# Kernel optimization log

Hardware: AMD Instinct MI355X
Metric: run time of the kernel (lower is better)

The kernel has to match this reference:

```python
import jax, jax.numpy as jnp
import numpy as np

E = 1024   # embedding_size
K = 64     # key_size
DH = 64    # head_size
H = 16     # layer_size (num heads)
F = 4096   # hidden_size
B, S = 4, 2048
EPS = float(np.finfo(np.float32).eps)  # torch RMSNorm default eps


def setup_inputs() -> dict:
    key = jax.random.key(0)
    ks = jax.random.split(key, 12)
    embeddings = jax.random.normal(ks[0], (B, S, E), dtype=jnp.float32)
    # causal additive mask: 0 on/below diagonal, -1e9 above
    tri = jnp.triu(jnp.ones((S, S), dtype=bool), k=1)
    causal_buffer = jnp.where(tri, -1e9, 0.0).astype(jnp.float32)[None]  # [1,S,S]
    # standard RoPE cos/sin buffers over the key dim
    inv_freq = 1.0 / (10000.0 ** (jnp.arange(0, K // 2, dtype=jnp.float32) * 2.0 / K))
    ang = jnp.arange(S, dtype=jnp.float32)[:, None] * inv_freq[None, :]  # [S,K/2]
    ang = jnp.concatenate([ang, ang], axis=-1)                           # [S,K]
    cos_buffer = jnp.cos(ang)[None]  # [1,S,K]
    sin_buffer = jnp.sin(ang)[None]
    sc = 0.02
    wq = jax.random.normal(ks[1], (H, E, K), dtype=jnp.float32) * sc
    wk = jax.random.normal(ks[2], (H, E, K), dtype=jnp.float32) * sc
    wv = jax.random.normal(ks[3], (H, E, DH), dtype=jnp.float32) * sc
    w_proj = jax.random.normal(ks[4], (E, E), dtype=jnp.float32) * sc
    attn_norm_w = jnp.ones((E,), dtype=jnp.float32)
    mlp_norm_w = jnp.ones((E,), dtype=jnp.float32)
    w_up = jax.random.normal(ks[5], (E, F), dtype=jnp.float32) * sc
    w_gate = jax.random.normal(ks[6], (E, F), dtype=jnp.float32) * sc
    w_down = jax.random.normal(ks[7], (F, E), dtype=jnp.float32) * sc
    return {"embeddings": embeddings, "causal_buffer": causal_buffer,
            "cos_buffer": cos_buffer, "sin_buffer": sin_buffer,
            "wq": wq, "wk": wk, "wv": wv, "w_proj": w_proj,
            "attn_norm_w": attn_norm_w, "mlp_norm_w": mlp_norm_w,
            "w_up": w_up, "w_gate": w_gate, "w_down": w_down}


def _rmsnorm(x, w):
    ms = jnp.mean(x * x, axis=-1, keepdims=True)
    return x * jax.lax.rsqrt(ms + EPS) * w


def _rotate(x, cos, sin):
    # x: [B,H,S,K]; cos/sin: [1,1,S,K]. swapped = cat(second_half, first_half)
    swapped = jnp.concatenate([x[..., K // 2:], x[..., :K // 2]], axis=-1)
    return cos * x + sin * swapped


def reference(embeddings, causal_buffer, cos_buffer, sin_buffer,
              wq, wk, wv, w_proj, attn_norm_w, mlp_norm_w,
              w_up, w_gate, w_down):
    cos = cos_buffer[:, None]  # [1,1,S,K]
    sin = sin_buffer[:, None]
    # NOTE: original computes attention_norm(embeddings) but feeds RAW
    # embeddings to the heads; we reproduce that faithfully.
    q = _rotate(jnp.einsum('bse,hek->bhsk', embeddings, wq), cos, sin)
    k = _rotate(jnp.einsum('bse,hek->bhsk', embeddings, wk), cos, sin)
    v = jnp.einsum('bse,hed->bhsd', embeddings, wv)
    scores = jnp.einsum('bhsk,bhtk->bhst', q, k) / jnp.sqrt(jnp.float32(K))
    scores = scores + causal_buffer[:, None]  # broadcast over heads
    weights = jax.nn.softmax(scores, axis=-1)
    attn = jnp.einsum('bhst,bhtd->bhsd', weights, v)  # [B,H,S,DH]
    attn = attn.transpose(0, 2, 1, 3).reshape(attn.shape[0], attn.shape[2], H * DH)
    x = embeddings + attn @ w_proj
    h = _rmsnorm(x, mlp_norm_w)
    mlp = (h @ w_up) * jax.nn.elu(h @ w_gate)
    return x + mlp @ w_down
```

## Files before the change

### kernel.cpp

```cpp
#include <hip/hip_runtime.h>
#include <cstdint>
#include <cstddef>

#define E_DIM 1024
#define S_LEN 2048
#define NB 4
#define NH 16
#define F_DIM 4096

typedef __attribute__((ext_vector_type(8))) __bf16 bf16x8;
typedef __attribute__((ext_vector_type(4))) __bf16 bf16x4;
typedef __attribute__((ext_vector_type(4))) float f32x4;

__device__ __forceinline__ f32x4 mfma16(bf16x8 a, bf16x8 b, f32x4 c) {
  return __builtin_amdgcn_mfma_f32_16x16x32_bf16(a, b, c, 0, 0, 0);
}

__device__ __forceinline__ unsigned short f2bf(float f) {
  __bf16 h = (__bf16)f;
  return __builtin_bit_cast(unsigned short, h);
}

__device__ __forceinline__ void gl_lds16(const void* gptr, void* lptr) {
  __builtin_amdgcn_global_load_lds(
      (const __attribute__((address_space(1))) void*)gptr,
      (__attribute__((address_space(3))) void*)lptr, 16, 0, 0);
}


__global__ __launch_bounds__(256) void cast_emb_kernel(
    const float4* __restrict__ in, ushort4* __restrict__ out) {
  int i = blockIdx.x * 256 + threadIdx.x;
  float4 v = in[i];
  ushort4 o;
  o.x = f2bf(v.x); o.y = f2bf(v.y); o.z = f2bf(v.z); o.w = f2bf(v.w);
  out[i] = o;
}

__global__ __launch_bounds__(256) void transpose_cast_kernel(
    const float* __restrict__ in, unsigned short* __restrict__ out, int R, int C) {
  __shared__ float tile[32][33];
  const int bz = blockIdx.z;
  const float* ip = in + (size_t)bz * R * C;
  const int r0 = blockIdx.y * 32, c0 = blockIdx.x * 32;
  const int tc = threadIdx.x & 31, tr = threadIdx.x >> 5;
#pragma unroll
  for (int i = 0; i < 4; ++i)
    tile[tr + i * 8][tc] = ip[(size_t)(r0 + tr + i * 8) * C + (c0 + tc)];
  __syncthreads();
#pragma unroll
  for (int i = 0; i < 4; ++i)
    out[(size_t)(bz * C + c0 + tr + i * 8) * R + (r0 + tc)] = f2bf(tile[tc][tr + i * 8]);
}

template <int EPI>
__global__ __launch_bounds__(256) void gemm_bt(
    const unsigned short* __restrict__ A, const unsigned short* __restrict__ Bt,
    int Kd, int N,
    const float* __restrict__ aux, const float* __restrict__ cosb,
    const float* __restrict__ sinb,
    unsigned short* __restrict__ qout, unsigned short* __restrict__ kout,
    unsigned short* __restrict__ vtout, float* __restrict__ fout) {
  __shared__ unsigned short As[128 * 32];
  __shared__ unsigned short Bs[128 * 32];
  const int t = threadIdx.x;
  const int lane = t & 63, w = t >> 6;
  const int quad = lane >> 4, l15 = lane & 15;
  const int wm = (w >> 1) * 64, wn = (w & 1) * 64;
  const int m0 = blockIdx.y * 128, n0 = blockIdx.x * 128;
  const int r = t >> 2, cb = (t & 3) * 8;
  const unsigned short* ga = A + (size_t)(m0 + r) * Kd + cb;
  const unsigned short* gb = Bt + (size_t)(n0 + r) * Kd + cb;
  unsigned short* lA0 = &As[r * 32 + cb];
  unsigned short* lA1 = &As[(r + 64) * 32 + cb];
  unsigned short* lB0 = &Bs[r * 32 + cb];
  unsigned short* lB1 = &Bs[(r + 64) * 32 + cb];
  f32x4 acc[4][4] = {};
  for (int k0 = 0; k0 < Kd; k0 += 32) {
    __syncthreads();
    gl_lds16(ga + k0, lA0);
    gl_lds16(ga + (size_t)64 * Kd + k0, lA1);
    gl_lds16(gb + k0, lB0);
    gl_lds16(gb + (size_t)64 * Kd + k0, lB1);
    __syncthreads();
    bf16x8 af[4], bfr[4];
#pragma unroll
    for (int mi = 0; mi < 4; ++mi)
      af[mi] = *reinterpret_cast<const bf16x8*>(&As[(wm + mi * 16 + l15) * 32 + quad * 8]);
#pragma unroll
    for (int ni = 0; ni < 4; ++ni)
      bfr[ni] = *reinterpret_cast<const bf16x8*>(&Bs[(wn + ni * 16 + l15) * 32 + quad * 8]);
#pragma unroll
    for (int mi = 0; mi < 4; ++mi)
#pragma unroll
      for (int ni = 0; ni < 4; ++ni)
        acc[mi][ni] = mfma16(af[mi], bfr[ni], acc[mi][ni]);
  }
  if (EPI == 0) {
#pragma unroll
    for (int mi = 0; mi < 4; ++mi) {
      const int mbase = m0 + wm + mi * 16 + quad * 4;
#pragma unroll
      for (int nt = 0; nt < 4; ++nt) {
        const int n = n0 + wn + nt * 16 + l15;
        const int seg = n >> 10, rest = n & 1023, hh = rest >> 6, kk = rest & 63;
#pragma unroll
        for (int rg = 0; rg < 4; ++rg) {
          const int m = mbase + rg;
          const int b = m >> 11, s = m & 2047;
          const float v = acc[mi][nt][rg];
          if (seg == 2) {
            vtout[(((size_t)(b * NH + hh)) * 64 + kk) * S_LEN + s] = f2bf(v);
          } else {
            const float sw = acc[mi][nt ^ 2][rg];
            const float cv = cosb[s * 64 + kk], sv = sinb[s * 64 + kk];
            const float scl = (seg == 0) ? 0.125f : 1.0f;
            unsigned short* dst = (seg == 0) ? qout : kout;
            dst[(((size_t)(b * NH + hh)) * S_LEN + s) * 64 + kk] = f2bf((cv * v + sv * sw) * scl);
          }
        }
      }
    }
  } else {
#pragma unroll
    for (int mi = 0; mi < 4; ++mi) {
      const int mbase = m0 + wm + mi * 16 + quad * 4;
#pragma unroll
      for (int nt = 0; nt < 4; ++nt) {
        const int n = n0 + wn + nt * 16 + l15;
#pragma unroll
        for (int rg = 0; rg < 4; ++rg) {
          const size_t idx = (size_t)(mbase + rg) * 1024 + n;
          fout[idx] = aux[idx] + acc[mi][nt][rg];
        }
      }
    }
  }
}

__global__ __launch_bounds__(256) void gemm_upgate(
    const unsigned short* __restrict__ A, const unsigned short* __restrict__ Bu,
    const unsigned short* __restrict__ Bg, unsigned short* __restrict__ gout) {
  __shared__ unsigned short As[128 * 32];
  __shared__ unsigned short Us[64 * 32];
  __shared__ unsigned short Gs[64 * 32];
  const int Kd = 1024;
  const int t = threadIdx.x;
  const int lane = t & 63, w = t >> 6;
  const int quad = lane >> 4, l15 = lane & 15;
  const int wm = (w >> 1) * 64, wn = (w & 1) * 32;
  const int m0 = blockIdx.y * 128, n0 = blockIdx.x * 64;
  const int r = t >> 2, cb = (t & 3) * 8;
  const unsigned short* ga = A + (size_t)(m0 + r) * Kd + cb;
  const unsigned short* gu = Bu + (size_t)(n0 + r) * Kd + cb;
  const unsigned short* gg = Bg + (size_t)(n0 + r) * Kd + cb;
  f32x4 au[4][2] = {}, ag[4][2] = {};
  for (int k0 = 0; k0 < Kd; k0 += 32) {
    __syncthreads();
    gl_lds16(ga + k0, &As[r * 32 + cb]);
    gl_lds16(ga + (size_t)64 * Kd + k0, &As[(r + 64) * 32 + cb]);
    gl_lds16(gu + k0, &Us[r * 32 + cb]);
    gl_lds16(gg + k0, &Gs[r * 32 + cb]);
    __syncthreads();
    bf16x8 af[4], bu[2], bg[2];
#pragma unroll
    for (int mi = 0; mi < 4; ++mi)
      af[mi] = *reinterpret_cast<const bf16x8*>(&As[(wm + mi * 16 + l15) * 32 + quad * 8]);
#pragma unroll
    for (int ni = 0; ni < 2; ++ni) {
      bu[ni] = *reinterpret_cast<const bf16x8*>(&Us[(wn + ni * 16 + l15) * 32 + quad * 8]);
      bg[ni] = *reinterpret_cast<const bf16x8*>(&Gs[(wn + ni * 16 + l15) * 32 + quad * 8]);
    }
#pragma unroll
    for (int mi = 0; mi < 4; ++mi)
#pragma unroll
      for (int ni = 0; ni < 2; ++ni) {
        au[mi][ni] = mfma16(af[mi], bu[ni], au[mi][ni]);
        ag[mi][ni] = mfma16(af[mi], bg[ni], ag[mi][ni]);
      }
  }
#pragma unroll
  for (int mi = 0; mi < 4; ++mi) {
    const int mbase = m0 + wm + mi * 16 + quad * 4;
#pragma unroll
    for (int ni = 0; ni < 2; ++ni) {
      const int n = n0 + wn + ni * 16 + l15;
#pragma unroll
      for (int rg = 0; rg < 4; ++rg) {
        const float u = au[mi][ni][rg], gt = ag[mi][ni][rg];
        const float e = gt > 0.f ? gt : (__expf(gt) - 1.f);
        gout[(size_t)(mbase + rg) * F_DIM + n] = f2bf(u * e);
      }
    }
  }
}

#define PS_STRIDE 68
__global__ __launch_bounds__(256) void flash_attn(
    const unsigned short* __restrict__ qb, const unsigned short* __restrict__ kb,
    const unsigned short* __restrict__ vtb, unsigned short* __restrict__ attn) {
  __shared__ unsigned short Ks[64 * 64];
  __shared__ unsigned short Vts[64 * 64];
  __shared__ unsigned short Ps[128 * PS_STRIDE];
  const int t = threadIdx.x, lane = t & 63, w = t >> 6;
  const int quad = lane >> 4, l15 = lane & 15;
  const int qt = 15 - blockIdx.y;
  const int bh = blockIdx.x;
  const int b = bh >> 4, hh = bh & 15;
  const unsigned short* qg = qb + (size_t)bh * S_LEN * 64;
  const unsigned short* kg = kb + (size_t)bh * S_LEN * 64;
  const unsigned short* vg = vtb + (size_t)bh * 64 * S_LEN;
  bf16x8 aq[2][2];
#pragma unroll
  for (int mi = 0; mi < 2; ++mi)
#pragma unroll
    for (int ks = 0; ks < 2; ++ks)
      aq[mi][ks] = *reinterpret_cast<const bf16x8*>(
          qg + (size_t)(qt * 128 + w * 32 + mi * 16 + l15) * 64 + ks * 32 + quad * 8);
  f32x4 o[2][4] = {};
  float lpart[2][4] = {};
  const int ktmax = 2 * qt + 1;
  for (int kt = 0; kt <= ktmax; ++kt) {
    __syncthreads();
    {
      const int rk = t >> 3, ck = (t & 7) * 8;
#pragma unroll
      for (int i = 0; i < 2; ++i) {
        gl_lds16(kg + (size_t)(kt * 64 + rk + i * 32) * 64 + ck, &Ks[(rk + i * 32) * 64 + ck]);
        gl_lds16(vg + (size_t)(rk + i * 32) * S_LEN + kt * 64 + ck, &Vts[(rk + i * 32) * 64 + ck]);
      }
    }
    __syncthreads();
    f32x4 sacc[2][4];
#pragma unroll
    for (int mi = 0; mi < 2; ++mi)
#pragma unroll
      for (int nt = 0; nt < 4; ++nt) sacc[mi][nt] = (f32x4){-8.f, -8.f, -8.f, -8.f};
#pragma unroll
    for (int nt = 0; nt < 4; ++nt) {
      bf16x8 b0 = *reinterpret_cast<const bf16x8*>(&Ks[(nt * 16 + l15) * 64 + quad * 8]);
      bf16x8 b1 = *reinterpret_cast<const bf16x8*>(&Ks[(nt * 16 + l15) * 64 + 32 + quad * 8]);
#pragma unroll
      for (int mi = 0; mi < 2; ++mi) {
        sacc[mi][nt] = mfma16(aq[mi][0], b0, sacc[mi][nt]);
        sacc[mi][nt] = mfma16(aq[mi][1], b1, sacc[mi][nt]);
      }
    }
    if (kt >= 2 * qt) {
#pragma unroll
      for (int mi = 0; mi < 2; ++mi)
#pragma unroll
        for (int nt = 0; nt < 4; ++nt)
#pragma unroll
          for (int rg = 0; rg < 4; ++rg) {
            const int row = qt * 128 + w * 32 + mi * 16 + quad * 4 + rg;
            const int col = kt * 64 + nt * 16 + l15;
            if (col > row) sacc[mi][nt][rg] = -1e9f;
          }
    }
#pragma unroll
    for (int mi = 0; mi < 2; ++mi)
#pragma unroll
      for (int nt = 0; nt < 4; ++nt)
#pragma unroll
        for (int rg = 0; rg < 4; ++rg) {
          const float p = __expf(sacc[mi][nt][rg]);
          lpart[mi][rg] += p;
          Ps[(w * 32 + mi * 16 + quad * 4 + rg) * PS_STRIDE + nt * 16 + l15] = f2bf(p);
        }
#pragma unroll
    for (int ks = 0; ks < 2; ++ks) {
      bf16x8 ap[2];
#pragma unroll
      for (int mi = 0; mi < 2; ++mi) {
        const unsigned short* pp =
            &Ps[(w * 32 + mi * 16 + l15) * PS_STRIDE + ks * 32 + quad * 8];
        bf16x4 lo = *reinterpret_cast<const bf16x4*>(pp);
        bf16x4 hi = *reinterpret_cast<const bf16x4*>(pp + 4);
        ap[mi] = __builtin_shufflevector(lo, hi, 0, 1, 2, 3, 4, 5, 6, 7);
      }
#pragma unroll
      for (int vt = 0; vt < 4; ++vt) {
        bf16x8 bv = *reinterpret_cast<const bf16x8*>(
            &Vts[(vt * 16 + l15) * 64 + ks * 32 + quad * 8]);
#pragma unroll
        for (int mi = 0; mi < 2; ++mi) o[mi][vt] = mfma16(ap[mi], bv, o[mi][vt]);
      }
    }
  }
  float linv[2][4];
#pragma unroll
  for (int mi = 0; mi < 2; ++mi)
#pragma unroll
    for (int rg = 0; rg < 4; ++rg) {
      float rs = lpart[mi][rg];
#pragma unroll
      for (int d = 1; d < 16; d <<= 1) rs += __shfl_xor(rs, d);
      linv[mi][rg] = 1.0f / rs;
    }
#pragma unroll
  for (int mi = 0; mi < 2; ++mi)
#pragma unroll
    for (int vt = 0; vt < 4; ++vt)
#pragma unroll
      for (int rg = 0; rg < 4; ++rg) {
        const int row = w * 32 + mi * 16 + quad * 4 + rg;
        const int s = qt * 128 + row;
        const float ov = o[mi][vt][rg] * linv[mi][rg];
        attn[((size_t)(b * S_LEN + s)) * E_DIM + hh * 64 + vt * 16 + l15] = f2bf(ov);
      }
}

__global__ __launch_bounds__(256) void rmsnorm_kernel(
    const float* __restrict__ x, const float* __restrict__ wgt,
    unsigned short* __restrict__ hout) {
  const int row = blockIdx.x;
  const int t = threadIdx.x;
  const float4 v = reinterpret_cast<const float4*>(x + (size_t)row * E_DIM)[t];
  float ss = v.x * v.x + v.y * v.y + v.z * v.z + v.w * v.w;
#pragma unroll
  for (int d = 1; d < 64; d <<= 1) ss += __shfl_xor(ss, d);
  __shared__ float red[4];
  if ((t & 63) == 0) red[t >> 6] = ss;
  __syncthreads();
  const float tot = red[0] + red[1] + red[2] + red[3];
  const float sc = rsqrtf(tot * (1.f / 1024.f) + 1.1920929e-07f);
  const float4 g = reinterpret_cast<const float4*>(wgt)[t];
  ushort4 ov;
  ov.x = f2bf(v.x * sc * g.x);
  ov.y = f2bf(v.y * sc * g.y);
  ov.z = f2bf(v.z * sc * g.z);
  ov.w = f2bf(v.w * sc * g.w);
  reinterpret_cast<ushort4*>(hout + (size_t)row * E_DIM)[t] = ov;
}

extern "C" void kernel_launch(void* const* d_in, const int* in_sizes, int n_in,
                              void* d_out, int out_size, void* d_ws, size_t ws_size,
                              hipStream_t stream) {
  (void)in_sizes; (void)n_in; (void)out_size; (void)ws_size;
  const float* emb = (const float*)d_in[0];
  const float* cosb = (const float*)d_in[2];
  const float* sinb = (const float*)d_in[3];
  const float* wq = (const float*)d_in[4];
  const float* wk = (const float*)d_in[5];
  const float* wv = (const float*)d_in[6];
  const float* wproj = (const float*)d_in[7];
  const float* mlpw = (const float*)d_in[9];
  const float* wup = (const float*)d_in[10];
  const float* wgate = (const float*)d_in[11];
  const float* wdown = (const float*)d_in[12];
  float* out = (float*)d_out;
  char* ws = (char*)d_ws;
  unsigned short* wqkv_t = (unsigned short*)(ws + 0);
  unsigned short* wproj_t = (unsigned short*)(ws + 6291456);
  unsigned short* wup_t = (unsigned short*)(ws + 8388608);
  unsigned short* wgate_t = (unsigned short*)(ws + 16777216);
  unsigned short* wdown_t = (unsigned short*)(ws + 25165824);
  unsigned short* embb = (unsigned short*)(ws + 33554432);
  unsigned short* qbuf = (unsigned short*)(ws + 50331648);
  unsigned short* kbuf = (unsigned short*)(ws + 67108864);
  unsigned short* vtbuf = (unsigned short*)(ws + 83886080);
  unsigned short* gbuf = (unsigned short*)(ws + 33554432);
  unsigned short* attnb = (unsigned short*)(ws + 100663296);
  float* xbuf = (float*)(ws + 117440512);
  unsigned short* hbuf = (unsigned short*)(ws + 150994944);

  dim3 blk(256);
  cast_emb_kernel<<<8192, blk, 0, stream>>>((const float4*)emb, (ushort4*)embb);
  transpose_cast_kernel<<<dim3(2, 32, 16), blk, 0, stream>>>(wq, wqkv_t, 1024, 64);
  transpose_cast_kernel<<<dim3(2, 32, 16), blk, 0, stream>>>(wk, wqkv_t + 1024 * 1024, 1024, 64);
  transpose_cast_kernel<<<dim3(2, 32, 16), blk, 0, stream>>>(wv, wqkv_t + 2048 * 1024, 1024, 64);
  transpose_cast_kernel<<<dim3(32, 32, 1), blk, 0, stream>>>(wproj, wproj_t, 1024, 1024);
  transpose_cast_kernel<<<dim3(128, 32, 1), blk, 0, stream>>>(wup, wup_t, 1024, 4096);
  transpose_cast_kernel<<<dim3(128, 32, 1), blk, 0, stream>>>(wgate, wgate_t, 1024, 4096);
  transpose_cast_kernel<<<dim3(32, 128, 1), blk, 0, stream>>>(wdown, wdown_t, 4096, 1024);
  gemm_bt<0><<<dim3(24, 64), blk, 0, stream>>>(embb, wqkv_t, 1024, 3072, nullptr, cosb,
                                               sinb, qbuf, kbuf, vtbuf, nullptr);
  flash_attn<<<dim3(64, 16), blk, 0, stream>>>(qbuf, kbuf, vtbuf, attnb);
  gemm_bt<1><<<dim3(8, 64), blk, 0, stream>>>(attnb, wproj_t, 1024, 1024, emb, nullptr,
                                              nullptr, nullptr, nullptr, nullptr, xbuf);
  rmsnorm_kernel<<<8192, blk, 0, stream>>>(xbuf, mlpw, hbuf);
  gemm_upgate<<<dim3(64, 64), blk, 0, stream>>>(hbuf, wup_t, wgate_t, gbuf);
  gemm_bt<2><<<dim3(8, 64), blk, 0, stream>>>(gbuf, wdown_t, 4096, 1024, xbuf, nullptr,
                                              nullptr, nullptr, nullptr, nullptr, out);
}
```

Before: 660.0 us.

## Widen GEMM K-tile to 64 and XOR-swizzle LDS layout in GEMMs and attention

The GEMM kernels now stage 64-wide K slices instead of 32, halving the number of barrier pairs per K loop. Global-to-LDS loads also use an XOR swizzle on 16-byte column chunks (global column permuted by row&7), and all LDS fragment reads apply the matching swizzle to avoid bank conflicts. The same swizzle is applied to the K and V^T tiles in the attention kernel. LDS use per block doubles for the GEMMs, which may reduce occupancy.

```diff
diff --git a/kernel.cpp b/kernel.cpp
--- a/kernel.cpp
+++ b/kernel.cpp
@@ -61,40 +61,46 @@
     const float* __restrict__ sinb,
     unsigned short* __restrict__ qout, unsigned short* __restrict__ kout,
     unsigned short* __restrict__ vtout, float* __restrict__ fout) {
-  __shared__ unsigned short As[128 * 32];
-  __shared__ unsigned short Bs[128 * 32];
+  __shared__ unsigned short As[128 * 64];
+  __shared__ unsigned short Bs[128 * 64];
   const int t = threadIdx.x;
   const int lane = t & 63, w = t >> 6;
   const int quad = lane >> 4, l15 = lane & 15;
   const int wm = (w >> 1) * 64, wn = (w & 1) * 64;
   const int m0 = blockIdx.y * 128, n0 = blockIdx.x * 128;
-  const int r = t >> 2, cb = (t & 3) * 8;
-  const unsigned short* ga = A + (size_t)(m0 + r) * Kd + cb;
-  const unsigned short* gb = Bt + (size_t)(n0 + r) * Kd + cb;
-  unsigned short* lA0 = &As[r * 32 + cb];
-  unsigned short* lA1 = &As[(r + 64) * 32 + cb];
-  unsigned short* lB0 = &Bs[r * 32 + cb];
-  unsigned short* lB1 = &Bs[(r + 64) * 32 + cb];
+  const int sr = t >> 3, sc = t & 7;
+  const int gcoff = (sc ^ (sr & 7)) * 8;
+  const unsigned short* ga = A + (size_t)(m0 + sr) * Kd + gcoff;
+  const unsigned short* gb = Bt + (size_t)(n0 + sr) * Kd + gcoff;
+  unsigned short* lA = &As[sr * 64 + sc * 8];
+  unsigned short* lB = &Bs[sr * 64 + sc * 8];
+  const int xh = l15 & 7;
   f32x4 acc[4][4] = {};
-  for (int k0 = 0; k0 < Kd; k0 += 32) {
-    __syncthreads();
-    gl_lds16(ga + k0, lA0);
-    gl_lds16(ga + (size_t)64 * Kd + k0, lA1);
-    gl_lds16(gb + k0, lB0);
-    gl_lds16(gb + (size_t)64 * Kd + k0, lB1);
-    __syncthreads();
-    bf16x8 af[4], bfr[4];
-#pragma unroll
-    for (int mi = 0; mi < 4; ++mi)
-      af[mi] = *reinterpret_cast<const bf16x8*>(&As[(wm + mi * 16 + l15) * 32 + quad * 8]);
-#pragma unroll
-    for (int ni = 0; ni < 4; ++ni)
-      bfr[ni] = *reinterpret_cast<const bf16x8*>(&Bs[(wn + ni * 16 + l15) * 32 + quad * 8]);
-#pragma unroll
-    for (int mi = 0; mi < 4; ++mi)
+  for (int k0 = 0; k0 < Kd; k0 += 64) {
+    __syncthreads();
+#pragma unroll
+    for (int i = 0; i < 4; ++i) {
+      gl_lds16(ga + (size_t)(i * 32) * Kd + k0, lA + i * 32 * 64);
+      gl_lds16(gb + (size_t)(i * 32) * Kd + k0, lB + i * 32 * 64);
+    }
+    __syncthreads();
+#pragma unroll
+    for (int ks = 0; ks < 2; ++ks) {
+      bf16x8 af[4], bfr[4];
+#pragma unroll
+      for (int mi = 0; mi < 4; ++mi)
+        af[mi] = *reinterpret_cast<const bf16x8*>(
+            &As[(wm + mi * 16 + l15) * 64 + (((ks * 4 + quad) ^ xh) * 8)]);
 #pragma unroll
       for (int ni = 0; ni < 4; ++ni)
-        acc[mi][ni] = mfma16(af[mi], bfr[ni], acc[mi][ni]);
+        bfr[ni] = *reinterpret_cast<const bf16x8*>(
+            &Bs[(wn + ni * 16 + l15) * 64 + (((ks * 4 + quad) ^ xh) * 8)]);
+#pragma unroll
+      for (int mi = 0; mi < 4; ++mi)
+#pragma unroll
+        for (int ni = 0; ni < 4; ++ni)
+          acc[mi][ni] = mfma16(af[mi], bfr[ni], acc[mi][ni]);
+    }
   }
   if (EPI == 0) {
 #pragma unroll
@@ -141,43 +147,56 @@
 __global__ __launch_bounds__(256) void gemm_upgate(
     const unsigned short* __restrict__ A, const unsigned short* __restrict__ Bu,
     const unsigned short* __restrict__ Bg, unsigned short* __restrict__ gout) {
-  __shared__ unsigned short As[128 * 32];
-  __shared__ unsigned short Us[64 * 32];
-  __shared__ unsigned short Gs[64 * 32];
+  __shared__ unsigned short As[128 * 64];
+  __shared__ unsigned short Us[64 * 64];
+  __shared__ unsigned short Gs[64 * 64];
   const int Kd = 1024;
   const int t = threadIdx.x;
   const int lane = t & 63, w = t >> 6;
   const int quad = lane >> 4, l15 = lane & 15;
   const int wm = (w >> 1) * 64, wn = (w & 1) * 32;
   const int m0 = blockIdx.y * 128, n0 = blockIdx.x * 64;
-  const int r = t >> 2, cb = (t & 3) * 8;
-  const unsigned short* ga = A + (size_t)(m0 + r) * Kd + cb;
-  const unsigned short* gu = Bu + (size_t)(n0 + r) * Kd + cb;
-  const unsigned short* gg = Bg + (size_t)(n0 + r) * Kd + cb;
+  const int sr = t >> 3, sc = t & 7;
+  const int gcoff = (sc ^ (sr & 7)) * 8;
+  const unsigned short* ga = A + (size_t)(m0 + sr) * Kd + gcoff;
+  const unsigned short* gu = Bu + (size_t)(n0 + sr) * Kd + gcoff;
+  const unsigned short* gg = Bg + (size_t)(n0 + sr) * Kd + gcoff;
+  unsigned short* lA = &As[sr * 64 + sc * 8];
+  unsigned short* lU = &Us[sr * 64 + sc * 8];
+  unsigned short* lG = &Gs[sr * 64 + sc * 8];
+  const int xh = l15 & 7;
   f32x4 au[4][2] = {}, ag[4][2] = {};
-  for (int k0 = 0; k0 < Kd; k0 += 32) {
-    __syncthreads();
-    gl_lds16(ga + k0, &As[r * 32 + cb]);
-    gl_lds16(ga + (size_t)64 * Kd + k0, &As[(r + 64) * 32 + cb]);
-    gl_lds16(gu + k0, &Us[r * 32 + cb]);
-    gl_lds16(gg + k0, &Gs[r * 32 + cb]);
-    __syncthreads();
-    bf16x8 af[4], bu[2], bg[2];
-#pragma unroll
-    for (int mi = 0; mi < 4; ++mi)
-      af[mi] = *reinterpret_cast<const bf16x8*>(&As[(wm + mi * 16 + l15) * 32 + quad * 8]);
-#pragma unroll
-    for (int ni = 0; ni < 2; ++ni) {
-      bu[ni] = *reinterpret_cast<const bf16x8*>(&Us[(wn + ni * 16 + l15) * 32 + quad * 8]);
-      bg[ni] = *reinterpret_cast<const bf16x8*>(&Gs[(wn + ni * 16 + l15) * 32 + quad * 8]);
-    }
-#pragma unroll
-    for (int mi = 0; mi < 4; ++mi)
+  for (int k0 = 0; k0 < Kd; k0 += 64) {
+    __syncthreads();
+#pragma unroll
+    for (int i = 0; i < 4; ++i)
+      gl_lds16(ga + (size_t)(i * 32) * Kd + k0, lA + i * 32 * 64);
+#pragma unroll
+    for (int i = 0; i < 2; ++i) {
+      gl_lds16(gu + (size_t)(i * 32) * Kd + k0, lU + i * 32 * 64);
+      gl_lds16(gg + (size_t)(i * 32) * Kd + k0, lG + i * 32 * 64);
+    }
+    __syncthreads();
+#pragma unroll
+    for (int ks = 0; ks < 2; ++ks) {
+      const int cp = ((ks * 4 + quad) ^ xh) * 8;
+      bf16x8 af[4], bu[2], bg[2];
+#pragma unroll
+      for (int mi = 0; mi < 4; ++mi)
+        af[mi] = *reinterpret_cast<const bf16x8*>(&As[(wm + mi * 16 + l15) * 64 + cp]);
 #pragma unroll
       for (int ni = 0; ni < 2; ++ni) {
-        au[mi][ni] = mfma16(af[mi], bu[ni], au[mi][ni]);
-        ag[mi][ni] = mfma16(af[mi], bg[ni], ag[mi][ni]);
-      }
+        bu[ni] = *reinterpret_cast<const bf16x8*>(&Us[(wn + ni * 16 + l15) * 64 + cp]);
+        bg[ni] = *reinterpret_cast<const bf16x8*>(&Gs[(wn + ni * 16 + l15) * 64 + cp]);
+      }
+#pragma unroll
+      for (int mi = 0; mi < 4; ++mi)
+#pragma unroll
+        for (int ni = 0; ni < 2; ++ni) {
+          au[mi][ni] = mfma16(af[mi], bu[ni], au[mi][ni]);
+          ag[mi][ni] = mfma16(af[mi], bg[ni], ag[mi][ni]);
+        }
+    }
   }
 #pragma unroll
   for (int mi = 0; mi < 4; ++mi) {
@@ -219,16 +238,18 @@
           qg + (size_t)(qt * 128 + w * 32 + mi * 16 + l15) * 64 + ks * 32 + quad * 8);
   f32x4 o[2][4] = {};
   float lpart[2][4] = {};
+  const int srk = t >> 3, sck = t & 7;
+  const int gck = ((sck ^ (srk & 7)) * 8);
+  const int xh = l15 & 7;
   const int ktmax = 2 * qt + 1;
   for (int kt = 0; kt <= ktmax; ++kt) {
     __syncthreads();
-    {
-      const int rk = t >> 3, ck = (t & 7) * 8;
-#pragma unroll
-      for (int i = 0; i < 2; ++i) {
-        gl_lds16(kg + (size_t)(kt * 64 + rk + i * 32) * 64 + ck, &Ks[(rk + i * 32) * 64 + ck]);
-        gl_lds16(vg + (size_t)(rk + i * 32) * S_LEN + kt * 64 + ck, &Vts[(rk + i * 32) * 64 + ck]);
-      }
+#pragma unroll
+    for (int i = 0; i < 2; ++i) {
+      gl_lds16(kg + (size_t)(kt * 64 + srk + i * 32) * 64 + gck,
+               &Ks[(srk + i * 32) * 64 + sck * 8]);
+      gl_lds16(vg + (size_t)(srk + i * 32) * S_LEN + kt * 64 + gck,
+               &Vts[(srk + i * 32) * 64 + sck * 8]);
     }
     __syncthreads();
     f32x4 sacc[2][4];
@@ -238,8 +259,10 @@
       for (int nt = 0; nt < 4; ++nt) sacc[mi][nt] = (f32x4){-8.f, -8.f, -8.f, -8.f};
 #pragma unroll
     for (int nt = 0; nt < 4; ++nt) {
-      bf16x8 b0 = *reinterpret_cast<const bf16x8*>(&Ks[(nt * 16 + l15) * 64 + quad * 8]);
-      bf16x8 b1 = *reinterpret_cast<const bf16x8*>(&Ks[(nt * 16 + l15) * 64 + 32 + quad * 8]);
+      bf16x8 b0 = *reinterpret_cast<const bf16x8*>(
+          &Ks[(nt * 16 + l15) * 64 + ((quad ^ xh) * 8)]);
+      bf16x8 b1 = *reinterpret_cast<const bf16x8*>(
+          &Ks[(nt * 16 + l15) * 64 + (((4 + quad) ^ xh) * 8)]);
 #pragma unroll
       for (int mi = 0; mi < 2; ++mi) {
         sacc[mi][nt] = mfma16(aq[mi][0], b0, sacc[mi][nt]);
@@ -282,7 +305,7 @@
 #pragma unroll
       for (int vt = 0; vt < 4; ++vt) {
         bf16x8 bv = *reinterpret_cast<const bf16x8*>(
-            &Vts[(vt * 16 + l15) * 64 + ks * 32 + quad * 8]);
+            &Vts[(vt * 16 + l15) * 64 + (((ks * 4 + quad) ^ xh) * 8)]);
 #pragma unroll
         for (int mi = 0; mi < 2; ++mi) o[mi][vt] = mfma16(ap[mi], bv, o[mi][vt]);
       }
```

Result: faster. 639.4 us (-3.1%).
